# Kernel optimization log

Measured on AMD Instinct MI355X. Metric: run time of the kernel, lower is better.

Reference implementation:

```python
import jax, jax.numpy as jnp
import numpy as np

NT, NH, NW = 16, 16, 16
HEADS, DIM_HEAD, DIM = 8, 64, 512


def setup_inputs() -> dict:
    key = jax.random.key(0)
    k1, k2 = jax.random.split(key)
    b, n = 8, NT * NH * NW
    x = jax.random.normal(k1, (b, n, DIM), dtype=jnp.float32)
    # torch Linear weight is [out,in]; store as [in,out] for x @ w
    w_qkv = jax.random.normal(k2, (DIM, 3 * HEADS * DIM_HEAD), dtype=jnp.float32) * 0.02
    return {"x": x, "w_qkv": w_qkv}


def _fd_attention(x, w_qkv):
    b, n, _ = x.shape
    h, d = HEADS, DIM_HEAD
    h2 = h // 2
    s = NH * NW  # spatial positions per frame
    scale = d ** -0.5

    qkv = x @ w_qkv  # [b, n, 3*h*d]
    q, k, v = jnp.split(qkv, 3, axis=-1)
    # 'b n (h d) -> b h n d'
    to_heads = lambda t: t.reshape(b, n, h, d).transpose(0, 2, 1, 3)
    q, k, v = to_heads(q), to_heads(k), to_heads(v)

    # first half of heads -> spatial attention (per frame, over nh*nw)
    qs = q[:, :h2].reshape(b, h2, NT, s, d)
    ks = k[:, :h2].reshape(b, h2, NT, s, d)
    vs = v[:, :h2].reshape(b, h2, NT, s, d)
    sp_dots = jnp.einsum('bhtid,bhtjd->bhtij', qs, ks) * scale
    sp_attn = jax.nn.softmax(sp_dots, axis=-1)
    spatial_out = jnp.einsum('bhtij,bhtjd->bhtid', sp_attn, vs)  # [b,h2,nt,s,d]

    # second half of heads -> temporal attention. NOTE: the original uses a raw
    # .view (not rearrange), reinterpreting the (nt*s) axis as (s, nt) in memory
    # order; we replicate that exact reshape semantics.
    qt = q[:, h2:].reshape(b, h2, s, NT, d)
    kt = k[:, h2:].reshape(b, h2, s, NT, d)
    vt = v[:, h2:].reshape(b, h2, s, NT, d)
    t_dots = jnp.einsum('bhsid,bhsjd->bhsij', qt, kt) * scale
    t_attn = jax.nn.softmax(t_dots, axis=-1)
    temporal_out = jnp.einsum('bhsij,bhsjd->bhsid', t_attn, vt)  # [b,h2,s,nt,d]

    # original forward ends here (no combine / to_out). Pack both branch outputs
    # flattened over tokens so the output is a single array: [2, b, h2, n, d]
    return jnp.stack([spatial_out.reshape(b, h2, n, d),
                      temporal_out.reshape(b, h2, n, d)], axis=0)


def reference(x, w_qkv):
    return _fd_attention(x, w_qkv)
```

## Files before the change

kernel.cpp:

```cpp
#include <hip/hip_runtime.h>
#include <math.h>

#define NBATCH 8
#define NTOK   4096
#define DIMX   512
#define QKVC   1536
#define DH     64
#define SCALE  0.125f

typedef __attribute__((ext_vector_type(8))) short short8;
typedef __attribute__((ext_vector_type(4))) float f32x4;


static __device__ __forceinline__ unsigned short f2bf_hi(float f) {
    unsigned u = __float_as_uint(f);
    return (unsigned short)((u + 0x8000u) >> 16);
}
static __device__ __forceinline__ unsigned short f2bf_lo(float f, unsigned short hi) {
    float hf = __uint_as_float(((unsigned)hi) << 16);
    return (unsigned short)(__float_as_uint(f - hf) >> 16);
}

#define BF_PACK2(H, L, F0, F1) do {                                             \
    unsigned short h0=f2bf_hi(F0.x),h1=f2bf_hi(F0.y),h2=f2bf_hi(F0.z),h3=f2bf_hi(F0.w); \
    unsigned short h4=f2bf_hi(F1.x),h5=f2bf_hi(F1.y),h6=f2bf_hi(F1.z),h7=f2bf_hi(F1.w); \
    H[0]=(short)h0; H[1]=(short)h1; H[2]=(short)h2; H[3]=(short)h3;             \
    H[4]=(short)h4; H[5]=(short)h5; H[6]=(short)h6; H[7]=(short)h7;             \
    L[0]=(short)f2bf_lo(F0.x,h0); L[1]=(short)f2bf_lo(F0.y,h1);                 \
    L[2]=(short)f2bf_lo(F0.z,h2); L[3]=(short)f2bf_lo(F0.w,h3);                 \
    L[4]=(short)f2bf_lo(F1.x,h4); L[5]=(short)f2bf_lo(F1.y,h5);                 \
    L[6]=(short)f2bf_lo(F1.z,h6); L[7]=(short)f2bf_lo(F1.w,h7);                 \
} while (0)

#define BF_PACKC(H, L, C) do {                                                  \
    unsigned short h0=f2bf_hi(lb0.C),h1=f2bf_hi(lb1.C),h2=f2bf_hi(lb2.C),h3=f2bf_hi(lb3.C); \
    unsigned short h4=f2bf_hi(lb4.C),h5=f2bf_hi(lb5.C),h6=f2bf_hi(lb6.C),h7=f2bf_hi(lb7.C); \
    H[0]=(short)h0; H[1]=(short)h1; H[2]=(short)h2; H[3]=(short)h3;             \
    H[4]=(short)h4; H[5]=(short)h5; H[6]=(short)h6; H[7]=(short)h7;             \
    L[0]=(short)f2bf_lo(lb0.C,h0); L[1]=(short)f2bf_lo(lb1.C,h1);               \
    L[2]=(short)f2bf_lo(lb2.C,h2); L[3]=(short)f2bf_lo(lb3.C,h3);               \
    L[4]=(short)f2bf_lo(lb4.C,h4); L[5]=(short)f2bf_lo(lb5.C,h5);               \
    L[6]=(short)f2bf_lo(lb6.C,h6); L[7]=(short)f2bf_lo(lb7.C,h7);               \
} while (0)

__global__ __launch_bounds__(256, 2) void qkv_gemm_mfma(const float* __restrict__ X,
                                                        const float* __restrict__ W,
                                                        float* __restrict__ QKV) {
    __shared__ short Ah[128 * 64];
    __shared__ short Al[128 * 64];
    __shared__ short Bh[128 * 64];
    __shared__ short Bl[128 * 64];

    const int t    = threadIdx.x;
    const int bm   = blockIdx.x & 255;
    const int bn   = blockIdx.x >> 8;
    const int m0   = bm * 128, n0 = bn * 128;
    const int lane = t & 63;
    const int wv   = t >> 6, wr = wv >> 1, wc = wv & 1;
    const int lr   = lane & 15, kg4 = lane >> 4;

    const int arow = t >> 1, ahalf = t & 1;
    const int bkg  = t & 7,  bcg   = t >> 3;

    f32x4 acc[4][4];
#pragma unroll
    for (int i = 0; i < 4; ++i)
#pragma unroll
        for (int j = 0; j < 4; ++j) acc[i][j] = (f32x4){0.f, 0.f, 0.f, 0.f};

    const float* Xp = X + (size_t)(m0 + arow) * DIMX + ahalf * 32;
    const float* Wp = W + (size_t)bkg * 8 * QKVC + n0 + bcg * 4;

    for (int k0 = 0; k0 < DIMX; k0 += 64) {
        float4 la0 = *(const float4*)(Xp + k0 +  0);
        float4 la1 = *(const float4*)(Xp + k0 +  4);
        float4 la2 = *(const float4*)(Xp + k0 +  8);
        float4 la3 = *(const float4*)(Xp + k0 + 12);
        float4 la4 = *(const float4*)(Xp + k0 + 16);
        float4 la5 = *(const float4*)(Xp + k0 + 20);
        float4 la6 = *(const float4*)(Xp + k0 + 24);
        float4 la7 = *(const float4*)(Xp + k0 + 28);
        const float* Wk = Wp + (size_t)k0 * QKVC;
        float4 lb0 = *(const float4*)(Wk + 0 * QKVC);
        float4 lb1 = *(const float4*)(Wk + 1 * QKVC);
        float4 lb2 = *(const float4*)(Wk + 2 * QKVC);
        float4 lb3 = *(const float4*)(Wk + 3 * QKVC);
        float4 lb4 = *(const float4*)(Wk + 4 * QKVC);
        float4 lb5 = *(const float4*)(Wk + 5 * QKVC);
        float4 lb6 = *(const float4*)(Wk + 6 * QKVC);
        float4 lb7 = *(const float4*)(Wk + 7 * QKVC);

        __syncthreads();

        {
            const int sw = (arow & 7) << 3;
            short8 H, L;
            BF_PACK2(H, L, la0, la1);
            { int idx = arow * 64 + ((ahalf * 32 +  0) ^ sw);
              *(short8*)&Ah[idx] = H; *(short8*)&Al[idx] = L; }
            BF_PACK2(H, L, la2, la3);
            { int idx = arow * 64 + ((ahalf * 32 +  8) ^ sw);
              *(short8*)&Ah[idx] = H; *(short8*)&Al[idx] = L; }
            BF_PACK2(H, L, la4, la5);
            { int idx = arow * 64 + ((ahalf * 32 + 16) ^ sw);
              *(short8*)&Ah[idx] = H; *(short8*)&Al[idx] = L; }
            BF_PACK2(H, L, la6, la7);
            { int idx = arow * 64 + ((ahalf * 32 + 24) ^ sw);
              *(short8*)&Ah[idx] = H; *(short8*)&Al[idx] = L; }
        }
        {
            short8 H, L;
            { int col = bcg * 4 + 0; int idx = col * 64 + ((bkg * 8) ^ ((col & 7) << 3));
              BF_PACKC(H, L, x); *(short8*)&Bh[idx] = H; *(short8*)&Bl[idx] = L; }
            { int col = bcg * 4 + 1; int idx = col * 64 + ((bkg * 8) ^ ((col & 7) << 3));
              BF_PACKC(H, L, y); *(short8*)&Bh[idx] = H; *(short8*)&Bl[idx] = L; }
            { int col = bcg * 4 + 2; int idx = col * 64 + ((bkg * 8) ^ ((col & 7) << 3));
              BF_PACKC(H, L, z); *(short8*)&Bh[idx] = H; *(short8*)&Bl[idx] = L; }
            { int col = bcg * 4 + 3; int idx = col * 64 + ((bkg * 8) ^ ((col & 7) << 3));
              BF_PACKC(H, L, w); *(short8*)&Bh[idx] = H; *(short8*)&Bl[idx] = L; }
        }
        __syncthreads();

#pragma unroll
        for (int ks = 0; ks < 2; ++ks) {
            short8 a_h[4], a_l[4], b_h[4], b_l[4];
#pragma unroll
            for (int fm = 0; fm < 4; ++fm) {
                int row = wr * 64 + fm * 16 + lr;
                int idx = row * 64 + ((ks * 32 + kg4 * 8) ^ ((row & 7) << 3));
                a_h[fm] = *(const short8*)&Ah[idx];
                a_l[fm] = *(const short8*)&Al[idx];
            }
#pragma unroll
            for (int fn = 0; fn < 4; ++fn) {
                int col = wc * 64 + fn * 16 + lr;
                int idx = col * 64 + ((ks * 32 + kg4 * 8) ^ ((col & 7) << 3));
                b_h[fn] = *(const short8*)&Bh[idx];
                b_l[fn] = *(const short8*)&Bl[idx];
            }
#pragma unroll
            for (int fm = 0; fm < 4; ++fm)
#pragma unroll
                for (int fn = 0; fn < 4; ++fn) {
                    acc[fm][fn] = __builtin_amdgcn_mfma_f32_16x16x32_bf16(
                        a_h[fm], b_h[fn], acc[fm][fn], 0, 0, 0);
                    acc[fm][fn] = __builtin_amdgcn_mfma_f32_16x16x32_bf16(
                        a_h[fm], b_l[fn], acc[fm][fn], 0, 0, 0);
                    acc[fm][fn] = __builtin_amdgcn_mfma_f32_16x16x32_bf16(
                        a_l[fm], b_h[fn], acc[fm][fn], 0, 0, 0);
                }
        }
    }

#pragma unroll
    for (int fm = 0; fm < 4; ++fm)
#pragma unroll
        for (int fn = 0; fn < 4; ++fn) {
            int col = n0 + wc * 64 + fn * 16 + lr;
#pragma unroll
            for (int j = 0; j < 4; ++j) {
                int row = m0 + wr * 64 + fm * 16 + kg4 * 4 + j;
                QKV[(size_t)row * QKVC + col] = acc[fm][fn][j];
            }
        }
}

#define QDOT(JJ, SREG) do {                                                     \
    const float* kr_ = &Ks[k0 + (JJ)][l16];                                     \
    float4 ka_ = *(const float4*)(kr_);      float4 kb_ = *(const float4*)(kr_ + 4);  \
    float4 kc_ = *(const float4*)(kr_ + 8);  float4 kd_ = *(const float4*)(kr_ + 12); \
    float d_ = qa.x * ka_.x;                                                    \
    d_ = fmaf(qa.y, ka_.y, d_); d_ = fmaf(qa.z, ka_.z, d_); d_ = fmaf(qa.w, ka_.w, d_); \
    d_ = fmaf(qb.x, kb_.x, d_); d_ = fmaf(qb.y, kb_.y, d_); d_ = fmaf(qb.z, kb_.z, d_); d_ = fmaf(qb.w, kb_.w, d_); \
    d_ = fmaf(qc.x, kc_.x, d_); d_ = fmaf(qc.y, kc_.y, d_); d_ = fmaf(qc.z, kc_.z, d_); d_ = fmaf(qc.w, kc_.w, d_); \
    d_ = fmaf(qd.x, kd_.x, d_); d_ = fmaf(qd.y, kd_.y, d_); d_ = fmaf(qd.z, kd_.z, d_); d_ = fmaf(qd.w, kd_.w, d_); \
    d_ += __shfl_xor(d_, 1, 4);  d_ += __shfl_xor(d_, 2, 4);                    \
    SREG = d_ * SCALE;                                                          \
} while (0)

#define PVACC(JJ, P) do {                                                       \
    const float* vr_ = &Vs[k0 + (JJ)][l16];                                     \
    float4 va_ = *(const float4*)(vr_);      float4 vb_ = *(const float4*)(vr_ + 4);  \
    float4 vc_ = *(const float4*)(vr_ + 8);  float4 vd_ = *(const float4*)(vr_ + 12); \
    ac0.x = fmaf((P), va_.x, ac0.x); ac0.y = fmaf((P), va_.y, ac0.y);           \
    ac0.z = fmaf((P), va_.z, ac0.z); ac0.w = fmaf((P), va_.w, ac0.w);           \
    ac1.x = fmaf((P), vb_.x, ac1.x); ac1.y = fmaf((P), vb_.y, ac1.y);           \
    ac1.z = fmaf((P), vb_.z, ac1.z); ac1.w = fmaf((P), vb_.w, ac1.w);           \
    ac2.x = fmaf((P), vc_.x, ac2.x); ac2.y = fmaf((P), vc_.y, ac2.y);           \
    ac2.z = fmaf((P), vc_.z, ac2.z); ac2.w = fmaf((P), vc_.w, ac2.w);           \
    ac3.x = fmaf((P), vd_.x, ac3.x); ac3.y = fmaf((P), vd_.y, ac3.y);           \
    ac3.z = fmaf((P), vd_.z, ac3.z); ac3.w = fmaf((P), vd_.w, ac3.w);           \
} while (0)

__global__ __launch_bounds__(1024, 1) void attn_spatial(const float* __restrict__ QKV,
                                                        float* __restrict__ Out) {
    __shared__ float Ks[256][DH];
    __shared__ float Vs[256][DH];
    const int t    = threadIdx.x;
    const int nt   = blockIdx.x & 15;
    const int h    = (blockIdx.x >> 4) & 3;
    const int b    = blockIdx.x >> 6;
    const int base = nt * 256;
    const int l16  = (t & 3) * 16;
    const int row  = t >> 2;
    const size_t rowoff = (size_t)b * NTOK;

    const float* Kg = QKV + (rowoff + base) * QKVC + 512  + h * DH;
    const float* Vg = QKV + (rowoff + base) * QKVC + 1024 + h * DH;
    const float* Qg = QKV + (rowoff + base + row) * QKVC + h * DH + l16;

#pragma unroll
    for (int i = 0; i < 4; ++i) {
        int idx = t + 1024 * i;
        int r = idx >> 4, c4 = (idx & 15) << 2;
        *(float4*)&Ks[r][c4] = *(const float4*)(Kg + (size_t)r * QKVC + c4);
        *(float4*)&Vs[r][c4] = *(const float4*)(Vg + (size_t)r * QKVC + c4);
    }

    float4 qa = *(const float4*)(Qg);
    float4 qb = *(const float4*)(Qg + 4);
    float4 qc = *(const float4*)(Qg + 8);
    float4 qd = *(const float4*)(Qg + 12);

    float4 ac0 = make_float4(0.f, 0.f, 0.f, 0.f);
    float4 ac1 = ac0, ac2 = ac0, ac3 = ac0;
    float m = -INFINITY, lsum = 0.f;

    __syncthreads();

    for (int k0 = 0; k0 < 256; k0 += 8) {
        float s0, s1, s2, s3, s4, s5, s6, s7;
        QDOT(0, s0); QDOT(1, s1); QDOT(2, s2); QDOT(3, s3);
        QDOT(4, s4); QDOT(5, s5); QDOT(6, s6); QDOT(7, s7);

        float cmax = fmaxf(fmaxf(fmaxf(s0, s1), fmaxf(s2, s3)),
                           fmaxf(fmaxf(s4, s5), fmaxf(s6, s7)));
        float mn   = fmaxf(m, cmax);
        float corr = __expf(m - mn);
        s0 = __expf(s0 - mn); s1 = __expf(s1 - mn); s2 = __expf(s2 - mn); s3 = __expf(s3 - mn);
        s4 = __expf(s4 - mn); s5 = __expf(s5 - mn); s6 = __expf(s6 - mn); s7 = __expf(s7 - mn);
        float psum = ((s0 + s1) + (s2 + s3)) + ((s4 + s5) + (s6 + s7));
        lsum = fmaf(lsum, corr, psum);
        m = mn;
        ac0.x *= corr; ac0.y *= corr; ac0.z *= corr; ac0.w *= corr;
        ac1.x *= corr; ac1.y *= corr; ac1.z *= corr; ac1.w *= corr;
        ac2.x *= corr; ac2.y *= corr; ac2.z *= corr; ac2.w *= corr;
        ac3.x *= corr; ac3.y *= corr; ac3.z *= corr; ac3.w *= corr;

        PVACC(0, s0); PVACC(1, s1); PVACC(2, s2); PVACC(3, s3);
        PVACC(4, s4); PVACC(5, s5); PVACC(6, s6); PVACC(7, s7);
    }

    float inv = 1.f / lsum;
    float* op = Out + ((size_t)(b * 4 + h) * NTOK + base + row) * DH + l16;
    *(float4*)(op)      = make_float4(ac0.x * inv, ac0.y * inv, ac0.z * inv, ac0.w * inv);
    *(float4*)(op + 4)  = make_float4(ac1.x * inv, ac1.y * inv, ac1.z * inv, ac1.w * inv);
    *(float4*)(op + 8)  = make_float4(ac2.x * inv, ac2.y * inv, ac2.z * inv, ac2.w * inv);
    *(float4*)(op + 12) = make_float4(ac3.x * inv, ac3.y * inv, ac3.z * inv, ac3.w * inv);
}

__global__ __launch_bounds__(256, 4) void attn_temporal(const float* __restrict__ QKV,
                                                        float* __restrict__ Out) {
    const int t    = threadIdx.x;
    const int l    = t & 3;
    const int row  = blockIdx.x * 64 + (t >> 2);
    const int tt   = row & 15;
    const int s    = (row >> 4) & 255;
    const int h    = (row >> 12) & 3;
    const int b    = row >> 14;
    const int head = 4 + h;
    const int token = s * 16 + tt;
    const size_t rowoff = (size_t)b * NTOK;

    const float* Qp = QKV + (rowoff + token) * QKVC + head * DH + l * 16;
    const float* Kb = QKV + (rowoff + s * 16) * QKVC + 512  + head * DH + l * 16;
    const float* Vb = QKV + (rowoff + s * 16) * QKVC + 1024 + head * DH + l * 16;

    float q[16];
#pragma unroll
    for (int c = 0; c < 16; c += 4) *(float4*)&q[c] = *(const float4*)(Qp + c);

    float sc[16];
    float mx = -INFINITY;
#pragma unroll
    for (int j = 0; j < 16; ++j) {
        const float* kr = Kb + (size_t)j * QKVC;
        float d = 0.f;
#pragma unroll
        for (int c = 0; c < 16; c += 4) {
            float4 kv = *(const float4*)(kr + c);
            d = fmaf(q[c], kv.x, d); d = fmaf(q[c+1], kv.y, d);
            d = fmaf(q[c+2], kv.z, d); d = fmaf(q[c+3], kv.w, d);
        }
        d += __shfl_xor(d, 1, 4);
        d += __shfl_xor(d, 2, 4);
        sc[j] = d * SCALE;
        mx = fmaxf(mx, sc[j]);
    }
    float lsum = 0.f;
#pragma unroll
    for (int j = 0; j < 16; ++j) { sc[j] = __expf(sc[j] - mx); lsum += sc[j]; }
    float inv = 1.f / lsum;

    float acc[16];
#pragma unroll
    for (int c = 0; c < 16; ++c) acc[c] = 0.f;
#pragma unroll
    for (int j = 0; j < 16; ++j) {
        const float* vr = Vb + (size_t)j * QKVC;
        float p = sc[j];
#pragma unroll
        for (int c = 0; c < 16; c += 4) {
            float4 vv = *(const float4*)(vr + c);
            acc[c]   = fmaf(p, vv.x, acc[c]);   acc[c+1] = fmaf(p, vv.y, acc[c+1]);
            acc[c+2] = fmaf(p, vv.z, acc[c+2]); acc[c+3] = fmaf(p, vv.w, acc[c+3]);
        }
    }
    float* op = Out + (size_t)(NBATCH * 4) * NTOK * DH
                    + ((size_t)(b * 4 + h) * NTOK + token) * DH + l * 16;
#pragma unroll
    for (int c = 0; c < 16; c += 4)
        *(float4*)(op + c) = make_float4(acc[c]*inv, acc[c+1]*inv, acc[c+2]*inv, acc[c+3]*inv);
}

extern "C" void kernel_launch(void* const* d_in, const int* in_sizes, int n_in,
                              void* d_out, int out_size, void* d_ws, size_t ws_size,
                              hipStream_t stream) {
    const float* x = (const float*)d_in[0];
    const float* w = (const float*)d_in[1];
    float* out = (float*)d_out;
    float* qkv = (float*)d_ws;

    qkv_gemm_mfma<<<dim3(3072), 256, 0, stream>>>(x, w, qkv);
    attn_spatial<<<dim3(512), 1024, 0, stream>>>(qkv, out);
    attn_temporal<<<dim3(2048), 256, 0, stream>>>(qkv, out);
}
```

Before: 623.4 us.

## Pre-split X into bf16 hi/lo planes and compute two query rows per spatial-attention thread

A new split_x kernel converts X once into bf16 high and low planes, staged in the output buffer as scratch. The GEMM then loads those planes directly instead of converting X in every column tile, where the same rows were converted 12 times. The spatial attention kernel now runs 512 threads per block, each handling two query rows, so every K/V element read from shared memory feeds twice the FMAs. The cost is an extra kernel launch with an extra pass over X, and higher register pressure in the attention kernel.

Measured after the change: 628.3 us. Within noise of the previous version (+0.8%).

```diff
diff --git a/kernel.cpp b/kernel.cpp
--- a/kernel.cpp
+++ b/kernel.cpp
@@ -10,7 +10,7 @@
 
 typedef __attribute__((ext_vector_type(8))) short short8;
 typedef __attribute__((ext_vector_type(4))) float f32x4;
-
+typedef __attribute__((ext_vector_type(4))) unsigned short us4;
 
 static __device__ __forceinline__ unsigned short f2bf_hi(float f) {
     unsigned u = __float_as_uint(f);
@@ -21,16 +21,17 @@
     return (unsigned short)(__float_as_uint(f - hf) >> 16);
 }
 
-#define BF_PACK2(H, L, F0, F1) do {                                             \
-    unsigned short h0=f2bf_hi(F0.x),h1=f2bf_hi(F0.y),h2=f2bf_hi(F0.z),h3=f2bf_hi(F0.w); \
-    unsigned short h4=f2bf_hi(F1.x),h5=f2bf_hi(F1.y),h6=f2bf_hi(F1.z),h7=f2bf_hi(F1.w); \
-    H[0]=(short)h0; H[1]=(short)h1; H[2]=(short)h2; H[3]=(short)h3;             \
-    H[4]=(short)h4; H[5]=(short)h5; H[6]=(short)h6; H[7]=(short)h7;             \
-    L[0]=(short)f2bf_lo(F0.x,h0); L[1]=(short)f2bf_lo(F0.y,h1);                 \
-    L[2]=(short)f2bf_lo(F0.z,h2); L[3]=(short)f2bf_lo(F0.w,h3);                 \
-    L[4]=(short)f2bf_lo(F1.x,h4); L[5]=(short)f2bf_lo(F1.y,h5);                 \
-    L[6]=(short)f2bf_lo(F1.z,h6); L[7]=(short)f2bf_lo(F1.w,h7);                 \
-} while (0)
+__global__ __launch_bounds__(256) void split_x(const float* __restrict__ X,
+                                               unsigned short* __restrict__ XH,
+                                               unsigned short* __restrict__ XL) {
+    size_t i = (size_t)blockIdx.x * 256 + threadIdx.x;
+    float4 v = *(const float4*)(X + i * 4);
+    unsigned short h0 = f2bf_hi(v.x), h1 = f2bf_hi(v.y), h2 = f2bf_hi(v.z), h3 = f2bf_hi(v.w);
+    us4 H = {h0, h1, h2, h3};
+    us4 L = {f2bf_lo(v.x, h0), f2bf_lo(v.y, h1), f2bf_lo(v.z, h2), f2bf_lo(v.w, h3)};
+    *(us4*)(XH + i * 4) = H;
+    *(us4*)(XL + i * 4) = L;
+}
 
 #define BF_PACKC(H, L, C) do {                                                  \
     unsigned short h0=f2bf_hi(lb0.C),h1=f2bf_hi(lb1.C),h2=f2bf_hi(lb2.C),h3=f2bf_hi(lb3.C); \
@@ -43,7 +44,8 @@
     L[6]=(short)f2bf_lo(lb6.C,h6); L[7]=(short)f2bf_lo(lb7.C,h7);               \
 } while (0)
 
-__global__ __launch_bounds__(256, 2) void qkv_gemm_mfma(const float* __restrict__ X,
+__global__ __launch_bounds__(256, 2) void qkv_gemm_mfma(const unsigned short* __restrict__ XH,
+                                                        const unsigned short* __restrict__ XL,
                                                         const float* __restrict__ W,
                                                         float* __restrict__ QKV) {
     __shared__ short Ah[128 * 64];
@@ -68,18 +70,19 @@
 #pragma unroll
         for (int j = 0; j < 4; ++j) acc[i][j] = (f32x4){0.f, 0.f, 0.f, 0.f};
 
-    const float* Xp = X + (size_t)(m0 + arow) * DIMX + ahalf * 32;
+    const unsigned short* XHp = XH + (size_t)(m0 + arow) * DIMX + ahalf * 32;
+    const unsigned short* XLp = XL + (size_t)(m0 + arow) * DIMX + ahalf * 32;
     const float* Wp = W + (size_t)bkg * 8 * QKVC + n0 + bcg * 4;
 
     for (int k0 = 0; k0 < DIMX; k0 += 64) {
-        float4 la0 = *(const float4*)(Xp + k0 +  0);
-        float4 la1 = *(const float4*)(Xp + k0 +  4);
-        float4 la2 = *(const float4*)(Xp + k0 +  8);
-        float4 la3 = *(const float4*)(Xp + k0 + 12);
-        float4 la4 = *(const float4*)(Xp + k0 + 16);
-        float4 la5 = *(const float4*)(Xp + k0 + 20);
-        float4 la6 = *(const float4*)(Xp + k0 + 24);
-        float4 la7 = *(const float4*)(Xp + k0 + 28);
+        short8 ha0 = *(const short8*)(XHp + k0 +  0);
+        short8 ha1 = *(const short8*)(XHp + k0 +  8);
+        short8 ha2 = *(const short8*)(XHp + k0 + 16);
+        short8 ha3 = *(const short8*)(XHp + k0 + 24);
+        short8 la0 = *(const short8*)(XLp + k0 +  0);
+        short8 la1 = *(const short8*)(XLp + k0 +  8);
+        short8 la2 = *(const short8*)(XLp + k0 + 16);
+        short8 la3 = *(const short8*)(XLp + k0 + 24);
         const float* Wk = Wp + (size_t)k0 * QKVC;
         float4 lb0 = *(const float4*)(Wk + 0 * QKVC);
         float4 lb1 = *(const float4*)(Wk + 1 * QKVC);
@@ -94,19 +97,14 @@
 
         {
             const int sw = (arow & 7) << 3;
-            short8 H, L;
-            BF_PACK2(H, L, la0, la1);
-            { int idx = arow * 64 + ((ahalf * 32 +  0) ^ sw);
-              *(short8*)&Ah[idx] = H; *(short8*)&Al[idx] = L; }
-            BF_PACK2(H, L, la2, la3);
-            { int idx = arow * 64 + ((ahalf * 32 +  8) ^ sw);
-              *(short8*)&Ah[idx] = H; *(short8*)&Al[idx] = L; }
-            BF_PACK2(H, L, la4, la5);
-            { int idx = arow * 64 + ((ahalf * 32 + 16) ^ sw);
-              *(short8*)&Ah[idx] = H; *(short8*)&Al[idx] = L; }
-            BF_PACK2(H, L, la6, la7);
-            { int idx = arow * 64 + ((ahalf * 32 + 24) ^ sw);
-              *(short8*)&Ah[idx] = H; *(short8*)&Al[idx] = L; }
+            int i0 = arow * 64 + ((ahalf * 32 +  0) ^ sw);
+            int i1 = arow * 64 + ((ahalf * 32 +  8) ^ sw);
+            int i2 = arow * 64 + ((ahalf * 32 + 16) ^ sw);
+            int i3 = arow * 64 + ((ahalf * 32 + 24) ^ sw);
+            *(short8*)&Ah[i0] = ha0; *(short8*)&Al[i0] = la0;
+            *(short8*)&Ah[i1] = ha1; *(short8*)&Al[i1] = la1;
+            *(short8*)&Ah[i2] = ha2; *(short8*)&Al[i2] = la2;
+            *(short8*)&Ah[i3] = ha3; *(short8*)&Al[i3] = la3;
         }
         {
             short8 H, L;
@@ -165,35 +163,49 @@
         }
 }
 
-#define QDOT(JJ, SREG) do {                                                     \
+#define QDOT2(JJ, SA, SB) do {                                                  \
     const float* kr_ = &Ks[k0 + (JJ)][l16];                                     \
-    float4 ka_ = *(const float4*)(kr_);      float4 kb_ = *(const float4*)(kr_ + 4);  \
-    float4 kc_ = *(const float4*)(kr_ + 8);  float4 kd_ = *(const float4*)(kr_ + 12); \
-    float d_ = qa.x * ka_.x;                                                    \
-    d_ = fmaf(qa.y, ka_.y, d_); d_ = fmaf(qa.z, ka_.z, d_); d_ = fmaf(qa.w, ka_.w, d_); \
-    d_ = fmaf(qb.x, kb_.x, d_); d_ = fmaf(qb.y, kb_.y, d_); d_ = fmaf(qb.z, kb_.z, d_); d_ = fmaf(qb.w, kb_.w, d_); \
-    d_ = fmaf(qc.x, kc_.x, d_); d_ = fmaf(qc.y, kc_.y, d_); d_ = fmaf(qc.z, kc_.z, d_); d_ = fmaf(qc.w, kc_.w, d_); \
-    d_ = fmaf(qd.x, kd_.x, d_); d_ = fmaf(qd.y, kd_.y, d_); d_ = fmaf(qd.z, kd_.z, d_); d_ = fmaf(qd.w, kd_.w, d_); \
-    d_ += __shfl_xor(d_, 1, 4);  d_ += __shfl_xor(d_, 2, 4);                    \
-    SREG = d_ * SCALE;                                                          \
+    float4 k0_ = *(const float4*)(kr_);      float4 k1_ = *(const float4*)(kr_ + 4);  \
+    float4 k2_ = *(const float4*)(kr_ + 8);  float4 k3_ = *(const float4*)(kr_ + 12); \
+    float dA_ = qa0.x * k0_.x;                                                  \
+    dA_ = fmaf(qa0.y, k0_.y, dA_); dA_ = fmaf(qa0.z, k0_.z, dA_); dA_ = fmaf(qa0.w, k0_.w, dA_); \
+    dA_ = fmaf(qb0.x, k1_.x, dA_); dA_ = fmaf(qb0.y, k1_.y, dA_); dA_ = fmaf(qb0.z, k1_.z, dA_); dA_ = fmaf(qb0.w, k1_.w, dA_); \
+    dA_ = fmaf(qc0.x, k2_.x, dA_); dA_ = fmaf(qc0.y, k2_.y, dA_); dA_ = fmaf(qc0.z, k2_.z, dA_); dA_ = fmaf(qc0.w, k2_.w, dA_); \
+    dA_ = fmaf(qd0.x, k3_.x, dA_); dA_ = fmaf(qd0.y, k3_.y, dA_); dA_ = fmaf(qd0.z, k3_.z, dA_); dA_ = fmaf(qd0.w, k3_.w, dA_); \
+    float dB_ = qa1.x * k0_.x;                                                  \
+    dB_ = fmaf(qa1.y, k0_.y, dB_); dB_ = fmaf(qa1.z, k0_.z, dB_); dB_ = fmaf(qa1.w, k0_.w, dB_); \
+    dB_ = fmaf(qb1.x, k1_.x, dB_); dB_ = fmaf(qb1.y, k1_.y, dB_); dB_ = fmaf(qb1.z, k1_.z, dB_); dB_ = fmaf(qb1.w, k1_.w, dB_); \
+    dB_ = fmaf(qc1.x, k2_.x, dB_); dB_ = fmaf(qc1.y, k2_.y, dB_); dB_ = fmaf(qc1.z, k2_.z, dB_); dB_ = fmaf(qc1.w, k2_.w, dB_); \
+    dB_ = fmaf(qd1.x, k3_.x, dB_); dB_ = fmaf(qd1.y, k3_.y, dB_); dB_ = fmaf(qd1.z, k3_.z, dB_); dB_ = fmaf(qd1.w, k3_.w, dB_); \
+    dA_ += __shfl_xor(dA_, 1, 4);  dA_ += __shfl_xor(dA_, 2, 4);                \
+    dB_ += __shfl_xor(dB_, 1, 4);  dB_ += __shfl_xor(dB_, 2, 4);                \
+    SA = dA_ * SCALE;  SB = dB_ * SCALE;                                        \
 } while (0)
 
-#define PVACC(JJ, P) do {                                                       \
+#define PV2(JJ, PA, PB) do {                                                    \
     const float* vr_ = &Vs[k0 + (JJ)][l16];                                     \
-    float4 va_ = *(const float4*)(vr_);      float4 vb_ = *(const float4*)(vr_ + 4);  \
-    float4 vc_ = *(const float4*)(vr_ + 8);  float4 vd_ = *(const float4*)(vr_ + 12); \
-    ac0.x = fmaf((P), va_.x, ac0.x); ac0.y = fmaf((P), va_.y, ac0.y);           \
-    ac0.z = fmaf((P), va_.z, ac0.z); ac0.w = fmaf((P), va_.w, ac0.w);           \
-    ac1.x = fmaf((P), vb_.x, ac1.x); ac1.y = fmaf((P), vb_.y, ac1.y);           \
-    ac1.z = fmaf((P), vb_.z, ac1.z); ac1.w = fmaf((P), vb_.w, ac1.w);           \
-    ac2.x = fmaf((P), vc_.x, ac2.x); ac2.y = fmaf((P), vc_.y, ac2.y);           \
-    ac2.z = fmaf((P), vc_.z, ac2.z); ac2.w = fmaf((P), vc_.w, ac2.w);           \
-    ac3.x = fmaf((P), vd_.x, ac3.x); ac3.y = fmaf((P), vd_.y, ac3.y);           \
-    ac3.z = fmaf((P), vd_.z, ac3.z); ac3.w = fmaf((P), vd_.w, ac3.w);           \
+    float4 v0_ = *(const float4*)(vr_);      float4 v1_ = *(const float4*)(vr_ + 4);  \
+    float4 v2_ = *(const float4*)(vr_ + 8);  float4 v3_ = *(const float4*)(vr_ + 12); \
+    aA0.x = fmaf((PA), v0_.x, aA0.x); aA0.y = fmaf((PA), v0_.y, aA0.y);         \
+    aA0.z = fmaf((PA), v0_.z, aA0.z); aA0.w = fmaf((PA), v0_.w, aA0.w);         \
+    aA1.x = fmaf((PA), v1_.x, aA1.x); aA1.y = fmaf((PA), v1_.y, aA1.y);         \
+    aA1.z = fmaf((PA), v1_.z, aA1.z); aA1.w = fmaf((PA), v1_.w, aA1.w);         \
+    aA2.x = fmaf((PA), v2_.x, aA2.x); aA2.y = fmaf((PA), v2_.y, aA2.y);         \
+    aA2.z = fmaf((PA), v2_.z, aA2.z); aA2.w = fmaf((PA), v2_.w, aA2.w);         \
+    aA3.x = fmaf((PA), v3_.x, aA3.x); aA3.y = fmaf((PA), v3_.y, aA3.y);         \
+    aA3.z = fmaf((PA), v3_.z, aA3.z); aA3.w = fmaf((PA), v3_.w, aA3.w);         \
+    aB0.x = fmaf((PB), v0_.x, aB0.x); aB0.y = fmaf((PB), v0_.y, aB0.y);         \
+    aB0.z = fmaf((PB), v0_.z, aB0.z); aB0.w = fmaf((PB), v0_.w, aB0.w);         \
+    aB1.x = fmaf((PB), v1_.x, aB1.x); aB1.y = fmaf((PB), v1_.y, aB1.y);         \
+    aB1.z = fmaf((PB), v1_.z, aB1.z); aB1.w = fmaf((PB), v1_.w, aB1.w);         \
+    aB2.x = fmaf((PB), v2_.x, aB2.x); aB2.y = fmaf((PB), v2_.y, aB2.y);         \
+    aB2.z = fmaf((PB), v2_.z, aB2.z); aB2.w = fmaf((PB), v2_.w, aB2.w);         \
+    aB3.x = fmaf((PB), v3_.x, aB3.x); aB3.y = fmaf((PB), v3_.y, aB3.y);         \
+    aB3.z = fmaf((PB), v3_.z, aB3.z); aB3.w = fmaf((PB), v3_.w, aB3.w);         \
 } while (0)
 
-__global__ __launch_bounds__(1024, 1) void attn_spatial(const float* __restrict__ QKV,
-                                                        float* __restrict__ Out) {
+__global__ __launch_bounds__(512) void attn_spatial(const float* __restrict__ QKV,
+                                                    float* __restrict__ Out) {
     __shared__ float Ks[256][DH];
     __shared__ float Vs[256][DH];
     const int t    = threadIdx.x;
@@ -202,61 +214,86 @@
     const int b    = blockIdx.x >> 6;
     const int base = nt * 256;
     const int l16  = (t & 3) * 16;
-    const int row  = t >> 2;
+    const int rp   = t >> 2;
     const size_t rowoff = (size_t)b * NTOK;
 
-    const float* Kg = QKV + (rowoff + base) * QKVC + 512  + h * DH;
-    const float* Vg = QKV + (rowoff + base) * QKVC + 1024 + h * DH;
-    const float* Qg = QKV + (rowoff + base + row) * QKVC + h * DH + l16;
-
-#pragma unroll
-    for (int i = 0; i < 4; ++i) {
-        int idx = t + 1024 * i;
+    const float* Kg  = QKV + (rowoff + base) * QKVC + 512  + h * DH;
+    const float* Vg  = QKV + (rowoff + base) * QKVC + 1024 + h * DH;
+    const float* QgA = QKV + (rowoff + base + rp) * QKVC + h * DH + l16;
+    const float* QgB = QKV + (rowoff + base + rp + 128) * QKVC + h * DH + l16;
+
+#pragma unroll
+    for (int i = 0; i < 8; ++i) {
+        int idx = t + 512 * i;
         int r = idx >> 4, c4 = (idx & 15) << 2;
         *(float4*)&Ks[r][c4] = *(const float4*)(Kg + (size_t)r * QKVC + c4);
         *(float4*)&Vs[r][c4] = *(const float4*)(Vg + (size_t)r * QKVC + c4);
     }
 
-    float4 qa = *(const float4*)(Qg);
-    float4 qb = *(const float4*)(Qg + 4);
-    float4 qc = *(const float4*)(Qg + 8);
-    float4 qd = *(const float4*)(Qg + 12);
-
-    float4 ac0 = make_float4(0.f, 0.f, 0.f, 0.f);
-    float4 ac1 = ac0, ac2 = ac0, ac3 = ac0;
-    float m = -INFINITY, lsum = 0.f;
+    float4 qa0 = *(const float4*)(QgA);      float4 qb0 = *(const float4*)(QgA + 4);
+    float4 qc0 = *(const float4*)(QgA + 8);  float4 qd0 = *(const float4*)(QgA + 12);
+    float4 qa1 = *(const float4*)(QgB);      float4 qb1 = *(const float4*)(QgB + 4);
+    float4 qc1 = *(const float4*)(QgB + 8);  float4 qd1 = *(const float4*)(QgB + 12);
+
+    float4 aA0 = make_float4(0.f, 0.f, 0.f, 0.f);
+    float4 aA1 = aA0, aA2 = aA0, aA3 = aA0;
+    float4 aB0 = aA0, aB1 = aA0, aB2 = aA0, aB3 = aA0;
+    float mA = -INFINITY, lA = 0.f, mB = -INFINITY, lB = 0.f;
 
     __syncthreads();
 
     for (int k0 = 0; k0 < 256; k0 += 8) {
-        float s0, s1, s2, s3, s4, s5, s6, s7;
-        QDOT(0, s0); QDOT(1, s1); QDOT(2, s2); QDOT(3, s3);
-        QDOT(4, s4); QDOT(5, s5); QDOT(6, s6); QDOT(7, s7);
-
-        float cmax = fmaxf(fmaxf(fmaxf(s0, s1), fmaxf(s2, s3)),
-                           fmaxf(fmaxf(s4, s5), fmaxf(s6, s7)));
-        float mn   = fmaxf(m, cmax);
-        float corr = __expf(m - mn);
-        s0 = __expf(s0 - mn); s1 = __expf(s1 - mn); s2 = __expf(s2 - mn); s3 = __expf(s3 - mn);
-        s4 = __expf(s4 - mn); s5 = __expf(s5 - mn); s6 = __expf(s6 - mn); s7 = __expf(s7 - mn);
-        float psum = ((s0 + s1) + (s2 + s3)) + ((s4 + s5) + (s6 + s7));
-        lsum = fmaf(lsum, corr, psum);
-        m = mn;
-        ac0.x *= corr; ac0.y *= corr; ac0.z *= corr; ac0.w *= corr;
-        ac1.x *= corr; ac1.y *= corr; ac1.z *= corr; ac1.w *= corr;
-        ac2.x *= corr; ac2.y *= corr; ac2.z *= corr; ac2.w *= corr;
-        ac3.x *= corr; ac3.y *= corr; ac3.z *= corr; ac3.w *= corr;
-
-        PVACC(0, s0); PVACC(1, s1); PVACC(2, s2); PVACC(3, s3);
-        PVACC(4, s4); PVACC(5, s5); PVACC(6, s6); PVACC(7, s7);
-    }
-
-    float inv = 1.f / lsum;
-    float* op = Out + ((size_t)(b * 4 + h) * NTOK + base + row) * DH + l16;
-    *(float4*)(op)      = make_float4(ac0.x * inv, ac0.y * inv, ac0.z * inv, ac0.w * inv);
-    *(float4*)(op + 4)  = make_float4(ac1.x * inv, ac1.y * inv, ac1.z * inv, ac1.w * inv);
-    *(float4*)(op + 8)  = make_float4(ac2.x * inv, ac2.y * inv, ac2.z * inv, ac2.w * inv);
-    *(float4*)(op + 12) = make_float4(ac3.x * inv, ac3.y * inv, ac3.z * inv, ac3.w * inv);
+        float sA0, sA1, sA2, sA3, sA4, sA5, sA6, sA7;
+        float sB0, sB1, sB2, sB3, sB4, sB5, sB6, sB7;
+        QDOT2(0, sA0, sB0); QDOT2(1, sA1, sB1); QDOT2(2, sA2, sB2); QDOT2(3, sA3, sB3);
+        QDOT2(4, sA4, sB4); QDOT2(5, sA5, sB5); QDOT2(6, sA6, sB6); QDOT2(7, sA7, sB7);
+
+        {
+            float cmax = fmaxf(fmaxf(fmaxf(sA0, sA1), fmaxf(sA2, sA3)),
+                               fmaxf(fmaxf(sA4, sA5), fmaxf(sA6, sA7)));
+            float mn   = fmaxf(mA, cmax);
+            float corr = __expf(mA - mn);
+            sA0 = __expf(sA0 - mn); sA1 = __expf(sA1 - mn); sA2 = __expf(sA2 - mn); sA3 = __expf(sA3 - mn);
+            sA4 = __expf(sA4 - mn); sA5 = __expf(sA5 - mn); sA6 = __expf(sA6 - mn); sA7 = __expf(sA7 - mn);
+            float ps = ((sA0 + sA1) + (sA2 + sA3)) + ((sA4 + sA5) + (sA6 + sA7));
+            lA = fmaf(lA, corr, ps);
+            mA = mn;
+            aA0.x *= corr; aA0.y *= corr; aA0.z *= corr; aA0.w *= corr;
+            aA1.x *= corr; aA1.y *= corr; aA1.z *= corr; aA1.w *= corr;
+            aA2.x *= corr; aA2.y *= corr; aA2.z *= corr; aA2.w *= corr;
+            aA3.x *= corr; aA3.y *= corr; aA3.z *= corr; aA3.w *= corr;
+        }
+        {
+            float cmax = fmaxf(fmaxf(fmaxf(sB0, sB1), fmaxf(sB2, sB3)),
+                               fmaxf(fmaxf(sB4, sB5), fmaxf(sB6, sB7)));
+            float mn   = fmaxf(mB, cmax);
+            float corr = __expf(mB - mn);
+            sB0 = __expf(sB0 - mn); sB1 = __expf(sB1 - mn); sB2 = __expf(sB2 - mn); sB3 = __expf(sB3 - mn);
+            sB4 = __expf(sB4 - mn); sB5 = __expf(sB5 - mn); sB6 = __expf(sB6 - mn); sB7 = __expf(sB7 - mn);
+            float ps = ((sB0 + sB1) + (sB2 + sB3)) + ((sB4 + sB5) + (sB6 + sB7));
+            lB = fmaf(lB, corr, ps);
+            mB = mn;
+            aB0.x *= corr; aB0.y *= corr; aB0.z *= corr; aB0.w *= corr;
+            aB1.x *= corr; aB1.y *= corr; aB1.z *= corr; aB1.w *= corr;
+            aB2.x *= corr; aB2.y *= corr; aB2.z *= corr; aB2.w *= corr;
+            aB3.x *= corr; aB3.y *= corr; aB3.z *= corr; aB3.w *= corr;
+        }
+
+        PV2(0, sA0, sB0); PV2(1, sA1, sB1); PV2(2, sA2, sB2); PV2(3, sA3, sB3);
+        PV2(4, sA4, sB4); PV2(5, sA5, sB5); PV2(6, sA6, sB6); PV2(7, sA7, sB7);
+    }
+
+    float invA = 1.f / lA, invB = 1.f / lB;
+    float* opA = Out + ((size_t)(b * 4 + h) * NTOK + base + rp) * DH + l16;
+    float* opB = Out + ((size_t)(b * 4 + h) * NTOK + base + rp + 128) * DH + l16;
+    *(float4*)(opA)      = make_float4(aA0.x*invA, aA0.y*invA, aA0.z*invA, aA0.w*invA);
+    *(float4*)(opA + 4)  = make_float4(aA1.x*invA, aA1.y*invA, aA1.z*invA, aA1.w*invA);
+    *(float4*)(opA + 8)  = make_float4(aA2.x*invA, aA2.y*invA, aA2.z*invA, aA2.w*invA);
+    *(float4*)(opA + 12) = make_float4(aA3.x*invA, aA3.y*invA, aA3.z*invA, aA3.w*invA);
+    *(float4*)(opB)      = make_float4(aB0.x*invB, aB0.y*invB, aB0.z*invB, aB0.w*invB);
+    *(float4*)(opB + 4)  = make_float4(aB1.x*invB, aB1.y*invB, aB1.z*invB, aB1.w*invB);
+    *(float4*)(opB + 8)  = make_float4(aB2.x*invB, aB2.y*invB, aB2.z*invB, aB2.w*invB);
+    *(float4*)(opB + 12) = make_float4(aB3.x*invB, aB3.y*invB, aB3.z*invB, aB3.w*invB);
 }
 
 __global__ __launch_bounds__(256, 4) void attn_temporal(const float* __restrict__ QKV,
@@ -331,7 +368,11 @@
     float* out = (float*)d_out;
     float* qkv = (float*)d_ws;
 
-    qkv_gemm_mfma<<<dim3(3072), 256, 0, stream>>>(x, w, qkv);
-    attn_spatial<<<dim3(512), 1024, 0, stream>>>(qkv, out);
+    unsigned short* xh = (unsigned short*)d_out;
+    unsigned short* xl = xh + (size_t)NBATCH * NTOK * DIMX;
+
+    split_x<<<dim3(16384), 256, 0, stream>>>(x, xh, xl);
+    qkv_gemm_mfma<<<dim3(3072), 256, 0, stream>>>(xh, xl, w, qkv);
+    attn_spatial<<<dim3(512), 512, 0, stream>>>(qkv, out);
     attn_temporal<<<dim3(2048), 256, 0, stream>>>(qkv, out);
 }
```
